# Optimization experiments

Measured on AMD Instinct MI355X. Metric: run time of the kernel, lower is better.

Reference implementation:

```python
import jax, jax.numpy as jnp
import numpy as np

BETA = 0.5
TAU_L = 0.1
TAU_H = 0.1
TOP_K = 2


def setup_inputs() -> dict:
    key = jax.random.key(0)
    ks = jax.random.split(key, 6)
    B, S, H, F, E, NH = 1, 2048, 1024, 3584, 8, 16
    hidden_states = jax.random.normal(ks[0], (B, S, H), dtype=jnp.float32)
    self_attn_weights = jax.random.uniform(ks[1], (B, NH, S, S), dtype=jnp.float32)
    gate_w = jax.random.normal(ks[2], (E, H), dtype=jnp.float32) * 0.02
    w1 = jax.random.normal(ks[3], (E, F, H), dtype=jnp.float32) * 0.02
    w2 = jax.random.normal(ks[4], (E, H, F), dtype=jnp.float32) * 0.02
    w3 = jax.random.normal(ks[5], (E, F, H), dtype=jnp.float32) * 0.02
    return {"hidden_states": hidden_states, "self_attn_weights": self_attn_weights,
            "gate_w": gate_w, "w1": w1, "w2": w2, "w3": w3}


def reference(hidden_states, self_attn_weights, gate_w, w1, w2, w3):
    B, S, H = hidden_states.shape
    E = gate_w.shape[0]
    x = hidden_states.reshape(-1, H)          # [T, H], T = B*S
    T = x.shape[0]

    router_logits = x @ gate_w.T              # [T, E]
    rw_full = jax.nn.softmax(router_logits.astype(jnp.float32), axis=-1)
    rw, sel = jax.lax.top_k(rw_full, TOP_K)   # [T, 2]

    # --- dynamic pruning branch (loss_index < block_range) ---
    mask_top1 = rw[:, 1] < BETA * rw[:, 0]
    new_routing = jnp.ones_like(rw)
    new_routing = new_routing.at[:, 1].set(jnp.where(mask_top1, 0.0, 1.0))

    # sequence_length > 1: attention-based token pruning (assumes B == 1)
    mean_tensor = jnp.mean(jnp.squeeze(self_attn_weights), axis=0)  # [S, S]
    column = mean_tensor.shape[1]
    real_number = jnp.arange(column, 0, -1, dtype=jnp.float32)
    attention_scores = jnp.sum(mean_tensor, axis=1) / real_number   # [S]
    l1_norm = jnp.sum(jnp.abs(x), axis=1)                           # [T]
    attention_scores = attention_scores * l1_norm

    n_low = int(TAU_L * T)
    n_high = int(TAU_H * T)
    _, low_idx = jax.lax.top_k(-attention_scores, n_low)   # smallest
    _, high_idx = jax.lax.top_k(attention_scores, n_high)  # largest
    mask_all = jnp.zeros((T,), dtype=bool).at[low_idx].set(True)
    keep_all = jnp.zeros((T,), dtype=bool).at[high_idx].set(True)
    new_routing = jnp.where(mask_all[:, None], 0.0, new_routing)
    new_routing = jnp.where(keep_all[:, None], 1.0, new_routing)

    rw = rw * new_routing
    denom = jnp.sum(rw, axis=-1, keepdims=True)
    rw = rw / jnp.where(denom > 0, denom, 1.0)  # fully-masked tokens -> 0 output
    rw = rw.astype(x.dtype)

    # combine weights per (token, expert); dispatch mask == new_routing
    cw = jnp.sum(rw[:, :, None] * jax.nn.one_hot(sel, E, dtype=rw.dtype), axis=1)  # [T, E]

    # dense reference for the gather-expert-scatter loop (SwiGLU experts)
    h = jnp.einsum('th,efh->tef', x, w1)      # [T, E, F]
    g = jnp.einsum('th,efh->tef', x, w3)
    a = jax.nn.silu(h) * g
    y = jnp.einsum('tef,ehf->teh', a, w2)     # [T, E, H]
    out = jnp.einsum('te,teh->th', cw, y)     # [T, H]

    return out.reshape(B, S, H), router_logits
```

## Files before the change

### kernel.cpp

```cpp
#include <hip/hip_runtime.h>
#include <hip/hip_bf16.h>
#include <math.h>

#define NTOK 2048
#define HDIM 1024
#define NEXP 8
#define FDIM 3584
#define NHEADS 16
#define NLOW 204
#define NHIGH 204
#define BK 32
#define LDST 40
#define KSPLIT 4
#define KCH (FDIM / KSPLIT)

typedef __bf16 bf16x8 __attribute__((ext_vector_type(8)));
typedef float f32x4 __attribute__((ext_vector_type(4)));

__global__ __launch_bounds__(256) void k_router(
    const float* __restrict__ x, const float* __restrict__ gw,
    float* __restrict__ logits, float* __restrict__ l1,
    int* __restrict__ sel0, int* __restrict__ sel1,
    float* __restrict__ rw0, float* __restrict__ rw1)
{
    __shared__ float sgw[NEXP * HDIM];
    int tid = threadIdx.x;
    for (int i = tid; i < NEXP * HDIM; i += 256) sgw[i] = gw[i];
    __syncthreads();
    int wv = tid >> 6, lane = tid & 63;
    int t = blockIdx.x * 4 + wv;
    const float* xr = x + (size_t)t * HDIM;
    float acc[NEXP];
#pragma unroll
    for (int e = 0; e < NEXP; ++e) acc[e] = 0.f;
    float al1 = 0.f;
    for (int h = lane; h < HDIM; h += 64) {
        float xv = xr[h];
        al1 += fabsf(xv);
#pragma unroll
        for (int e = 0; e < NEXP; ++e) acc[e] += xv * sgw[e * HDIM + h];
    }
#pragma unroll
    for (int off = 32; off > 0; off >>= 1) {
#pragma unroll
        for (int e = 0; e < NEXP; ++e) acc[e] += __shfl_xor(acc[e], off);
        al1 += __shfl_xor(al1, off);
    }
    if (lane < NEXP) logits[t * NEXP + lane] = acc[lane];
    if (lane == 0) {
        l1[t] = al1;
        float m = acc[0];
#pragma unroll
        for (int e = 1; e < NEXP; ++e) m = fmaxf(m, acc[e]);
        float p[NEXP], s = 0.f;
#pragma unroll
        for (int e = 0; e < NEXP; ++e) { p[e] = expf(acc[e] - m); s += p[e]; }
        float inv = 1.f / s;
        float b0 = -1.f, b1 = -1.f; int i0 = 0, i1 = 0;
#pragma unroll
        for (int e = 0; e < NEXP; ++e) {
            float r = p[e] * inv;
            if (r > b0) { b1 = b0; i1 = i0; b0 = r; i0 = e; }
            else if (r > b1) { b1 = r; i1 = e; }
        }
        sel0[t] = i0; sel1[t] = i1; rw0[t] = b0; rw1[t] = b1;
    }
}

__global__ __launch_bounds__(256) void k_attn(
    const float* __restrict__ attn, const float* __restrict__ l1,
    float* __restrict__ scores)
{
    int i = blockIdx.x, tid = threadIdx.x;
    float acc = 0.f;
    for (int h = 0; h < NHEADS; ++h) {
        const float4* p = (const float4*)(attn + ((size_t)h * NTOK + i) * NTOK);
        for (int j = tid; j < NTOK / 4; j += 256) {
            float4 v = p[j];
            acc += v.x + v.y + v.z + v.w;
        }
    }
    __shared__ float red[256];
    red[tid] = acc; __syncthreads();
    for (int s = 128; s > 0; s >>= 1) {
        if (tid < s) red[tid] += red[tid + s];
        __syncthreads();
    }
    if (tid == 0) scores[i] = red[0] / (16.f * (float)(NTOK - i)) * l1[i];
}

__global__ __launch_bounds__(256) void k_rank(
    const float* __restrict__ scores, const float* __restrict__ rw0,
    const float* __restrict__ rw1, float* __restrict__ w0f, float* __restrict__ w1f)
{
    __shared__ float s[NTOK];
    int tid = threadIdx.x;
    for (int i = tid; i < NTOK; i += 256) s[i] = scores[i];
    __syncthreads();
    int t = blockIdx.x * 256 + tid;
    float st = s[t];
    int cl = 0, ch = 0;
    for (int j = 0; j < NTOK; ++j) {
        float sj = s[j];
        int tie = (sj == st) && (j < t);
        cl += (sj < st) || tie;
        ch += (sj > st) || tie;
    }
    bool in_low = cl < NLOW, keep = ch < NHIGH;
    float a = rw0[t], b = rw1[t];
    float n0 = 1.f, n1 = (b < 0.5f * a) ? 0.f : 1.f;
    if (in_low) { n0 = 0.f; n1 = 0.f; }
    if (keep)   { n0 = 1.f; n1 = 1.f; }
    a *= n0; b *= n1;
    float d = a + b;
    if (d > 0.f) { a /= d; b /= d; }
    w0f[t] = a; w1f[t] = b;
}

__global__ __launch_bounds__(512) void k_build(
    const int* __restrict__ sel0, const int* __restrict__ sel1,
    const float* __restrict__ w0f, const float* __restrict__ w1f,
    int* __restrict__ tok, float* __restrict__ wgt,
    int* __restrict__ counts, int* __restrict__ offs)
{
    int tid = threadIdx.x;
    int e = tid >> 6, lane = tid & 63;
    unsigned long long below = (1ull << lane) - 1ull;
    int base = 0;
    for (int r = 0; r < NTOK / 64; ++r) {
        int t = r * 64 + lane;
        bool f0 = (sel0[t] == e) && (w0f[t] > 0.f);
        unsigned long long m0 = __ballot(f0);
        if (f0) {
            int pos = base + __popcll(m0 & below);
            tok[e * NTOK + pos] = t; wgt[e * NTOK + pos] = w0f[t];
        }
        base += __popcll(m0);
        bool f1 = (sel1[t] == e) && (w1f[t] > 0.f);
        unsigned long long m1 = __ballot(f1);
        if (f1) {
            int pos = base + __popcll(m1 & below);
            tok[e * NTOK + pos] = t; wgt[e * NTOK + pos] = w1f[t];
        }
        base += __popcll(m1);
    }
    if (lane == 0) counts[e] = base;
    __syncthreads();
    if (tid == 0) {
        int o = 0;
        for (int i = 0; i < NEXP; ++i) { offs[i] = o; o += counts[i]; }
    }
}

__global__ __launch_bounds__(256) void k_zero(float4* __restrict__ out)
{
    out[blockIdx.x * 256 + threadIdx.x] = make_float4(0.f, 0.f, 0.f, 0.f);
}

struct F16v { float4 a, b, c, d; };
__device__ inline F16v ld16(const float* __restrict__ p)
{
    F16v v;
    v.a = *(const float4*)p;
    v.b = *(const float4*)(p + 4);
    v.c = *(const float4*)(p + 8);
    v.d = *(const float4*)(p + 12);
    return v;
}
__device__ inline void st16(__hip_bfloat16* dst, const F16v& v)
{
    bf16x8 lo, hi;
    lo[0] = (__bf16)v.a.x; lo[1] = (__bf16)v.a.y; lo[2] = (__bf16)v.a.z; lo[3] = (__bf16)v.a.w;
    lo[4] = (__bf16)v.b.x; lo[5] = (__bf16)v.b.y; lo[6] = (__bf16)v.b.z; lo[7] = (__bf16)v.b.w;
    hi[0] = (__bf16)v.c.x; hi[1] = (__bf16)v.c.y; hi[2] = (__bf16)v.c.z; hi[3] = (__bf16)v.c.w;
    hi[4] = (__bf16)v.d.x; hi[5] = (__bf16)v.d.y; hi[6] = (__bf16)v.d.z; hi[7] = (__bf16)v.d.w;
    *(bf16x8*)dst = lo;
    *(bf16x8*)(dst + 8) = hi;
}

__global__ __launch_bounds__(256, 2) void k_ffn1(
    const float* __restrict__ x, const float* __restrict__ w1,
    const float* __restrict__ w3,
    const int* __restrict__ tok, const float* __restrict__ wgt,
    const int* __restrict__ counts, const int* __restrict__ offs,
    __hip_bfloat16* __restrict__ act)
{
    int e = blockIdx.z;
    int cnt = counts[e];
    int m0 = blockIdx.y * 128;
    if (m0 >= cnt) return;
    int f0 = blockIdx.x * 128;
    int tid = threadIdx.x;
    __shared__ __align__(16) __hip_bfloat16 sX[2][128 * LDST];
    __shared__ __align__(16) __hip_bfloat16 sW1[2][128 * LDST];
    __shared__ __align__(16) __hip_bfloat16 sW3[2][128 * LDST];
    __shared__ int sTok[128];
    __shared__ float sWgt[128];
    if (tid < 128) {
        int row = m0 + tid;
        int rr = (row < cnt) ? row : (cnt - 1);
        sTok[tid] = tok[e * NTOK + rr];
        sWgt[tid] = (row < cnt) ? wgt[e * NTOK + row] : 0.f;
    }
    __syncthreads();

    int r = tid >> 1, c16 = (tid & 1) * 16;
    const float* xp  = x  + (size_t)sTok[r] * HDIM + c16;
    const float* w1p = w1 + ((size_t)e * FDIM + f0 + r) * HDIM + c16;
    const float* w3p = w3 + ((size_t)e * FDIM + f0 + r) * HDIM + c16;
    int sidx = r * LDST + c16;

    F16v va = ld16(xp), vb = ld16(w1p), vc = ld16(w3p);
    st16(&sX[0][sidx], va); st16(&sW1[0][sidx], vb); st16(&sW3[0][sidx], vc);
    __syncthreads();

    int wv = tid >> 6, lane = tid & 63;
    int wm = (wv >> 1) * 64, wf = (wv & 1) * 64;
    int col = lane & 15, kfrag = (lane >> 4) * 8;
    f32x4 acc1[4][4] = {}, acc3[4][4] = {};
    int cur = 0;
    for (int k0 = 0; k0 < HDIM; k0 += BK) {
        bool more = (k0 + BK) < HDIM;
        if (more) {
            va = ld16(xp + k0 + BK);
            vb = ld16(w1p + k0 + BK);
            vc = ld16(w3p + k0 + BK);
        }
        bf16x8 af[4], b1[4], b3[4];
#pragma unroll
        for (int m = 0; m < 4; ++m)
            af[m] = *(const bf16x8*)&sX[cur][(wm + m * 16 + col) * LDST + kfrag];
#pragma unroll
        for (int f = 0; f < 4; ++f) {
            b1[f] = *(const bf16x8*)&sW1[cur][(wf + f * 16 + col) * LDST + kfrag];
            b3[f] = *(const bf16x8*)&sW3[cur][(wf + f * 16 + col) * LDST + kfrag];
        }
#pragma unroll
        for (int m = 0; m < 4; ++m)
#pragma unroll
            for (int f = 0; f < 4; ++f) {
                acc1[m][f] = __builtin_amdgcn_mfma_f32_16x16x32_bf16(af[m], b1[f], acc1[m][f], 0, 0, 0);
                acc3[m][f] = __builtin_amdgcn_mfma_f32_16x16x32_bf16(af[m], b3[f], acc3[m][f], 0, 0, 0);
            }
        if (more) {
            st16(&sX[cur ^ 1][sidx], va);
            st16(&sW1[cur ^ 1][sidx], vb);
            st16(&sW3[cur ^ 1][sidx], vc);
        }
        __syncthreads();
        cur ^= 1;
    }
    int soff = offs[e];
#pragma unroll
    for (int m = 0; m < 4; ++m) {
        int mb = wm + m * 16 + (lane >> 4) * 4;
#pragma unroll
        for (int q = 0; q < 4; ++q) {
            int rloc = mb + q;
            if (m0 + rloc < cnt) {
                float wgtv = sWgt[rloc];
#pragma unroll
                for (int f = 0; f < 4; ++f) {
                    float hv = acc1[m][f][q], gv = acc3[m][f][q];
                    float av = hv / (1.f + expf(-hv)) * gv * wgtv;
                    act[(size_t)(soff + m0 + rloc) * FDIM + f0 + wf + f * 16 + col] =
                        (__hip_bfloat16)av;
                }
            }
        }
    }
}

__global__ __launch_bounds__(256, 3) void k_ffn2(
    const __hip_bfloat16* __restrict__ act, const float* __restrict__ w2,
    const int* __restrict__ tok, const int* __restrict__ counts,
    const int* __restrict__ offs, float* __restrict__ out)
{
    int z = blockIdx.z;
    int e = z >> 2;
    int kbase = (z & 3) * KCH;
    int cnt = counts[e];
    int m0 = blockIdx.y * 128;
    if (m0 >= cnt) return;
    int h0 = blockIdx.x * 128;
    int tid = threadIdx.x;
    __shared__ __align__(16) __hip_bfloat16 sA[2][128 * LDST];
    __shared__ __align__(16) __hip_bfloat16 sB[2][128 * LDST];
    __shared__ int sTok[128];
    if (tid < 128) {
        int row = m0 + tid;
        sTok[tid] = (row < cnt) ? tok[e * NTOK + row] : 0;
    }
    __syncthreads();
    int soff = offs[e];
    int r = tid >> 1, c16 = (tid & 1) * 16;
    int arow = (m0 + r < cnt) ? (m0 + r) : (cnt - 1);
    const __hip_bfloat16* ap = act + (size_t)(soff + arow) * FDIM + kbase + c16;
    const float* bp = w2 + ((size_t)e * HDIM + h0 + r) * FDIM + kbase + c16;
    int sidx = r * LDST + c16;

    bf16x8 a0 = *(const bf16x8*)ap, a1 = *(const bf16x8*)(ap + 8);
    F16v vb = ld16(bp);
    *(bf16x8*)&sA[0][sidx] = a0; *(bf16x8*)&sA[0][sidx + 8] = a1;
    st16(&sB[0][sidx], vb);
    __syncthreads();

    int wv = tid >> 6, lane = tid & 63;
    int wm = (wv >> 1) * 64, wh = (wv & 1) * 64;
    int col = lane & 15, kfrag = (lane >> 4) * 8;
    f32x4 acc[4][4] = {};
    int cur = 0;
    for (int k0 = 0; k0 < KCH; k0 += BK) {
        bool more = (k0 + BK) < KCH;
        if (more) {
            a0 = *(const bf16x8*)(ap + k0 + BK);
            a1 = *(const bf16x8*)(ap + k0 + BK + 8);
            vb = ld16(bp + k0 + BK);
        }
        bf16x8 aa[4], bb[4];
#pragma unroll
        for (int m = 0; m < 4; ++m)
            aa[m] = *(const bf16x8*)&sA[cur][(wm + m * 16 + col) * LDST + kfrag];
#pragma unroll
        for (int f = 0; f < 4; ++f)
            bb[f] = *(const bf16x8*)&sB[cur][(wh + f * 16 + col) * LDST + kfrag];
#pragma unroll
        for (int m = 0; m < 4; ++m)
#pragma unroll
            for (int f = 0; f < 4; ++f)
                acc[m][f] = __builtin_amdgcn_mfma_f32_16x16x32_bf16(aa[m], bb[f], acc[m][f], 0, 0, 0);
        if (more) {
            *(bf16x8*)&sA[cur ^ 1][sidx] = a0;
            *(bf16x8*)&sA[cur ^ 1][sidx + 8] = a1;
            st16(&sB[cur ^ 1][sidx], vb);
        }
        __syncthreads();
        cur ^= 1;
    }
#pragma unroll
    for (int m = 0; m < 4; ++m) {
        int mb = wm + m * 16 + (lane >> 4) * 4;
#pragma unroll
        for (int q = 0; q < 4; ++q) {
            int rloc = mb + q;
            if (m0 + rloc < cnt) {
                int t = sTok[rloc];
#pragma unroll
                for (int f = 0; f < 4; ++f)
                    atomicAdd(&out[(size_t)t * HDIM + h0 + wh + f * 16 + col], acc[m][f][q]);
            }
        }
    }
}

extern "C" void kernel_launch(void* const* d_in, const int* in_sizes, int n_in,
                              void* d_out, int out_size, void* d_ws, size_t ws_size,
                              hipStream_t stream)
{
    const float* x    = (const float*)d_in[0];
    const float* attn = (const float*)d_in[1];
    const float* gw   = (const float*)d_in[2];
    const float* w1   = (const float*)d_in[3];
    const float* w2   = (const float*)d_in[4];
    const float* w3   = (const float*)d_in[5];
    float* out = (float*)d_out;
    float* logits = out + (size_t)NTOK * HDIM;

    char* ws = (char*)d_ws;
    float* l1     = (float*)(ws + 0);
    float* scores = (float*)(ws + 8192);
    int*   sel0   = (int*)(ws + 16384);
    int*   sel1   = (int*)(ws + 24576);
    float* rw0    = (float*)(ws + 32768);
    float* rw1    = (float*)(ws + 40960);
    float* w0f    = (float*)(ws + 49152);
    float* w1f    = (float*)(ws + 57344);
    int*   counts = (int*)(ws + 65536);
    int*   offs   = (int*)(ws + 65600);
    int*   tok    = (int*)(ws + 73728);
    float* wgt    = (float*)(ws + 143360);
    __hip_bfloat16* act = (__hip_bfloat16*)(ws + 1048576);

    k_router<<<NTOK / 4, 256, 0, stream>>>(x, gw, logits, l1, sel0, sel1, rw0, rw1);
    k_attn<<<NTOK, 256, 0, stream>>>(attn, l1, scores);
    k_rank<<<NEXP, 256, 0, stream>>>(scores, rw0, rw1, w0f, w1f);
    k_build<<<1, 512, 0, stream>>>(sel0, sel1, w0f, w1f, tok, wgt, counts, offs);
    k_zero<<<NTOK, 256, 0, stream>>>((float4*)out);
    k_ffn1<<<dim3(FDIM / 128, NTOK / 128, NEXP), 256, 0, stream>>>(
        x, w1, w3, tok, wgt, counts, offs, act);
    k_ffn2<<<dim3(HDIM / 128, NTOK / 128, NEXP * KSPLIT), 256, 0, stream>>>(
        act, w2, tok, counts, offs, out);
}
```

Before: 408.4 us.

## Pre-convert activations to bf16 and deepen global-load prefetch in expert GEMMs

Adds a kernel that converts hidden states to bf16 once, so the FFN1 gather loads half the bytes and skips per-tile conversion. Both FFN GEMMs now keep two K-tiles of global loads in flight (a register ping-pong) instead of one, to hide memory latency. The launch grid of k_rank also changes. The deeper prefetch raises register pressure under the two-blocks-per-CU launch bound and may cause spills.

Result: slower. 550.0 us (+34.7%).

```diff
diff --git a/kernel.cpp b/kernel.cpp
--- a/kernel.cpp
+++ b/kernel.cpp
@@ -17,6 +17,18 @@
 typedef __bf16 bf16x8 __attribute__((ext_vector_type(8)));
 typedef float f32x4 __attribute__((ext_vector_type(4)));
 
+__global__ __launch_bounds__(256) void k_xbf16(
+    const float* __restrict__ x, __hip_bfloat16* __restrict__ xb)
+{
+    int i = (blockIdx.x * 256 + threadIdx.x) * 8;
+    float4 a = *(const float4*)(x + i);
+    float4 b = *(const float4*)(x + i + 4);
+    bf16x8 v;
+    v[0] = (__bf16)a.x; v[1] = (__bf16)a.y; v[2] = (__bf16)a.z; v[3] = (__bf16)a.w;
+    v[4] = (__bf16)b.x; v[5] = (__bf16)b.y; v[6] = (__bf16)b.z; v[7] = (__bf16)b.w;
+    *(bf16x8*)(xb + i) = v;
+}
+
 __global__ __launch_bounds__(256) void k_router(
     const float* __restrict__ x, const float* __restrict__ gw,
     float* __restrict__ logits, float* __restrict__ l1,
@@ -179,7 +191,7 @@
 }
 
 __global__ __launch_bounds__(256, 2) void k_ffn1(
-    const float* __restrict__ x, const float* __restrict__ w1,
+    const __hip_bfloat16* __restrict__ xb, const float* __restrict__ w1,
     const float* __restrict__ w3,
     const int* __restrict__ tok, const float* __restrict__ wgt,
     const int* __restrict__ counts, const int* __restrict__ offs,
@@ -205,47 +217,76 @@
     __syncthreads();
 
     int r = tid >> 1, c16 = (tid & 1) * 16;
-    const float* xp  = x  + (size_t)sTok[r] * HDIM + c16;
+    const __hip_bfloat16* xp = xb + (size_t)sTok[r] * HDIM + c16;
     const float* w1p = w1 + ((size_t)e * FDIM + f0 + r) * HDIM + c16;
     const float* w3p = w3 + ((size_t)e * FDIM + f0 + r) * HDIM + c16;
     int sidx = r * LDST + c16;
 
-    F16v va = ld16(xp), vb = ld16(w1p), vc = ld16(w3p);
-    st16(&sX[0][sidx], va); st16(&sW1[0][sidx], vb); st16(&sW3[0][sidx], vc);
+    {
+        bf16x8 x0 = *(const bf16x8*)xp, x1 = *(const bf16x8*)(xp + 8);
+        F16v w0 = ld16(w1p), g0 = ld16(w3p);
+        *(bf16x8*)&sX[0][sidx] = x0;
+        *(bf16x8*)&sX[0][sidx + 8] = x1;
+        st16(&sW1[0][sidx], w0);
+        st16(&sW3[0][sidx], g0);
+    }
+    bf16x8 xB0 = *(const bf16x8*)(xp + BK), xB1 = *(const bf16x8*)(xp + BK + 8);
+    F16v wB = ld16(w1p + BK), gB = ld16(w3p + BK);
     __syncthreads();
 
     int wv = tid >> 6, lane = tid & 63;
     int wm = (wv >> 1) * 64, wf = (wv & 1) * 64;
     int col = lane & 15, kfrag = (lane >> 4) * 8;
     f32x4 acc1[4][4] = {}, acc3[4][4] = {};
+
+    auto compute = [&](int bufi) {
+        bf16x8 af[4], b1f[4], b3f[4];
+#pragma unroll
+        for (int m = 0; m < 4; ++m)
+            af[m] = *(const bf16x8*)&sX[bufi][(wm + m * 16 + col) * LDST + kfrag];
+#pragma unroll
+        for (int f = 0; f < 4; ++f) {
+            b1f[f] = *(const bf16x8*)&sW1[bufi][(wf + f * 16 + col) * LDST + kfrag];
+            b3f[f] = *(const bf16x8*)&sW3[bufi][(wf + f * 16 + col) * LDST + kfrag];
+        }
+#pragma unroll
+        for (int m = 0; m < 4; ++m)
+#pragma unroll
+            for (int f = 0; f < 4; ++f) {
+                acc1[m][f] = __builtin_amdgcn_mfma_f32_16x16x32_bf16(af[m], b1f[f], acc1[m][f], 0, 0, 0);
+                acc3[m][f] = __builtin_amdgcn_mfma_f32_16x16x32_bf16(af[m], b3f[f], acc3[m][f], 0, 0, 0);
+            }
+    };
+
+    bf16x8 xA0, xA1; F16v wA, gA;
     int cur = 0;
-    for (int k0 = 0; k0 < HDIM; k0 += BK) {
-        bool more = (k0 + BK) < HDIM;
-        if (more) {
-            va = ld16(xp + k0 + BK);
-            vb = ld16(w1p + k0 + BK);
-            vc = ld16(w3p + k0 + BK);
-        }
-        bf16x8 af[4], b1[4], b3[4];
-#pragma unroll
-        for (int m = 0; m < 4; ++m)
-            af[m] = *(const bf16x8*)&sX[cur][(wm + m * 16 + col) * LDST + kfrag];
-#pragma unroll
-        for (int f = 0; f < 4; ++f) {
-            b1[f] = *(const bf16x8*)&sW1[cur][(wf + f * 16 + col) * LDST + kfrag];
-            b3[f] = *(const bf16x8*)&sW3[cur][(wf + f * 16 + col) * LDST + kfrag];
-        }
-#pragma unroll
-        for (int m = 0; m < 4; ++m)
-#pragma unroll
-            for (int f = 0; f < 4; ++f) {
-                acc1[m][f] = __builtin_amdgcn_mfma_f32_16x16x32_bf16(af[m], b1[f], acc1[m][f], 0, 0, 0);
-                acc3[m][f] = __builtin_amdgcn_mfma_f32_16x16x32_bf16(af[m], b3[f], acc3[m][f], 0, 0, 0);
-            }
-        if (more) {
-            st16(&sX[cur ^ 1][sidx], va);
-            st16(&sW1[cur ^ 1][sidx], vb);
-            st16(&sW3[cur ^ 1][sidx], vc);
+    for (int i = 0; i < HDIM / BK; i += 2) {
+        const int kc = i * BK;
+        if (i + 2 < HDIM / BK) {
+            xA0 = *(const bf16x8*)(xp + kc + 2 * BK);
+            xA1 = *(const bf16x8*)(xp + kc + 2 * BK + 8);
+            wA = ld16(w1p + kc + 2 * BK);
+            gA = ld16(w3p + kc + 2 * BK);
+        }
+        compute(cur);
+        *(bf16x8*)&sX[cur ^ 1][sidx] = xB0;
+        *(bf16x8*)&sX[cur ^ 1][sidx + 8] = xB1;
+        st16(&sW1[cur ^ 1][sidx], wB);
+        st16(&sW3[cur ^ 1][sidx], gB);
+        __syncthreads();
+        cur ^= 1;
+        if (i + 3 < HDIM / BK) {
+            xB0 = *(const bf16x8*)(xp + kc + 3 * BK);
+            xB1 = *(const bf16x8*)(xp + kc + 3 * BK + 8);
+            wB = ld16(w1p + kc + 3 * BK);
+            gB = ld16(w3p + kc + 3 * BK);
+        }
+        compute(cur);
+        if (i + 2 < HDIM / BK) {
+            *(bf16x8*)&sX[cur ^ 1][sidx] = xA0;
+            *(bf16x8*)&sX[cur ^ 1][sidx + 8] = xA1;
+            st16(&sW1[cur ^ 1][sidx], wA);
+            st16(&sW3[cur ^ 1][sidx], gA);
         }
         __syncthreads();
         cur ^= 1;
@@ -299,40 +340,62 @@
     const float* bp = w2 + ((size_t)e * HDIM + h0 + r) * FDIM + kbase + c16;
     int sidx = r * LDST + c16;
 
-    bf16x8 a0 = *(const bf16x8*)ap, a1 = *(const bf16x8*)(ap + 8);
-    F16v vb = ld16(bp);
-    *(bf16x8*)&sA[0][sidx] = a0; *(bf16x8*)&sA[0][sidx + 8] = a1;
-    st16(&sB[0][sidx], vb);
+    {
+        bf16x8 a0 = *(const bf16x8*)ap, a1 = *(const bf16x8*)(ap + 8);
+        F16v b0 = ld16(bp);
+        *(bf16x8*)&sA[0][sidx] = a0;
+        *(bf16x8*)&sA[0][sidx + 8] = a1;
+        st16(&sB[0][sidx], b0);
+    }
+    bf16x8 aB0 = *(const bf16x8*)(ap + BK), aB1 = *(const bf16x8*)(ap + BK + 8);
+    F16v wB = ld16(bp + BK);
     __syncthreads();
 
     int wv = tid >> 6, lane = tid & 63;
     int wm = (wv >> 1) * 64, wh = (wv & 1) * 64;
     int col = lane & 15, kfrag = (lane >> 4) * 8;
     f32x4 acc[4][4] = {};
-    int cur = 0;
-    for (int k0 = 0; k0 < KCH; k0 += BK) {
-        bool more = (k0 + BK) < KCH;
-        if (more) {
-            a0 = *(const bf16x8*)(ap + k0 + BK);
-            a1 = *(const bf16x8*)(ap + k0 + BK + 8);
-            vb = ld16(bp + k0 + BK);
-        }
+
+    auto compute = [&](int bufi) {
         bf16x8 aa[4], bb[4];
 #pragma unroll
         for (int m = 0; m < 4; ++m)
-            aa[m] = *(const bf16x8*)&sA[cur][(wm + m * 16 + col) * LDST + kfrag];
+            aa[m] = *(const bf16x8*)&sA[bufi][(wm + m * 16 + col) * LDST + kfrag];
 #pragma unroll
         for (int f = 0; f < 4; ++f)
-            bb[f] = *(const bf16x8*)&sB[cur][(wh + f * 16 + col) * LDST + kfrag];
+            bb[f] = *(const bf16x8*)&sB[bufi][(wh + f * 16 + col) * LDST + kfrag];
 #pragma unroll
         for (int m = 0; m < 4; ++m)
 #pragma unroll
             for (int f = 0; f < 4; ++f)
                 acc[m][f] = __builtin_amdgcn_mfma_f32_16x16x32_bf16(aa[m], bb[f], acc[m][f], 0, 0, 0);
-        if (more) {
-            *(bf16x8*)&sA[cur ^ 1][sidx] = a0;
-            *(bf16x8*)&sA[cur ^ 1][sidx + 8] = a1;
-            st16(&sB[cur ^ 1][sidx], vb);
+    };
+
+    bf16x8 aA0, aA1; F16v wA;
+    int cur = 0;
+    for (int i = 0; i < KCH / BK; i += 2) {
+        const int kc = i * BK;
+        if (i + 2 < KCH / BK) {
+            aA0 = *(const bf16x8*)(ap + kc + 2 * BK);
+            aA1 = *(const bf16x8*)(ap + kc + 2 * BK + 8);
+            wA = ld16(bp + kc + 2 * BK);
+        }
+        compute(cur);
+        *(bf16x8*)&sA[cur ^ 1][sidx] = aB0;
+        *(bf16x8*)&sA[cur ^ 1][sidx + 8] = aB1;
+        st16(&sB[cur ^ 1][sidx], wB);
+        __syncthreads();
+        cur ^= 1;
+        if (i + 3 < KCH / BK) {
+            aB0 = *(const bf16x8*)(ap + kc + 3 * BK);
+            aB1 = *(const bf16x8*)(ap + kc + 3 * BK + 8);
+            wB = ld16(bp + kc + 3 * BK);
+        }
+        compute(cur);
+        if (i + 2 < KCH / BK) {
+            *(bf16x8*)&sA[cur ^ 1][sidx] = aA0;
+            *(bf16x8*)&sA[cur ^ 1][sidx + 8] = aA1;
+            st16(&sB[cur ^ 1][sidx], wA);
         }
         __syncthreads();
         cur ^= 1;
@@ -380,14 +443,16 @@
     int*   tok    = (int*)(ws + 73728);
     float* wgt    = (float*)(ws + 143360);
     __hip_bfloat16* act = (__hip_bfloat16*)(ws + 1048576);
-
+    __hip_bfloat16* xb  = (__hip_bfloat16*)(ws + 33554432);
+
+    k_xbf16<<<NTOK * HDIM / (256 * 8), 256, 0, stream>>>(x, xb);
     k_router<<<NTOK / 4, 256, 0, stream>>>(x, gw, logits, l1, sel0, sel1, rw0, rw1);
     k_attn<<<NTOK, 256, 0, stream>>>(attn, l1, scores);
-    k_rank<<<NEXP, 256, 0, stream>>>(scores, rw0, rw1, w0f, w1f);
+    k_rank<<<NTOK / 256, 256, 0, stream>>>(scores, rw0, rw1, w0f, w1f);
     k_build<<<1, 512, 0, stream>>>(sel0, sel1, w0f, w1f, tok, wgt, counts, offs);
     k_zero<<<NTOK, 256, 0, stream>>>((float4*)out);
     k_ffn1<<<dim3(FDIM / 128, NTOK / 128, NEXP), 256, 0, stream>>>(
-        x, w1, w3, tok, wgt, counts, offs, act);
+        xb, w1, w3, tok, wgt, counts, offs, act);
     k_ffn2<<<dim3(HDIM / 128, NTOK / 128, NEXP * KSPLIT), 256, 0, stream>>>(
         act, w2, tok, counts, offs, out);
 }
```

## Split fused gate/up GEMM into two kernels and pre-convert x to bf16

Applied to the files above, without the earlier changes.

Splits the fused w1/w3 expert GEMM into two kernels, k_h and k_g, each with a single accumulator set and a single weight tile. This lowers register and LDS pressure so launch bounds can rise from 2 to 3 blocks per SM. The up kernel writes h to a bf16 buffer that the gate kernel reads back in its SiLU epilogue. x is converted to bf16 once up front, so gathered token rows are loaded as bf16 and each x tile is loaded twice instead of once. This adds an extra kernel launch and an h round trip through global memory. The k_rank grid also changes from NEXP to NTOK/256, which is the same value (8).

Result: slower. 474.9 us (+16.3%).

```diff
diff --git a/kernel.cpp b/kernel.cpp
--- a/kernel.cpp
+++ b/kernel.cpp
@@ -17,6 +17,18 @@
 typedef __bf16 bf16x8 __attribute__((ext_vector_type(8)));
 typedef float f32x4 __attribute__((ext_vector_type(4)));
 
+__global__ __launch_bounds__(256) void k_xbf16(
+    const float* __restrict__ x, __hip_bfloat16* __restrict__ xb)
+{
+    int i = (blockIdx.x * 256 + threadIdx.x) * 8;
+    float4 a = *(const float4*)(x + i);
+    float4 b = *(const float4*)(x + i + 4);
+    bf16x8 v;
+    v[0] = (__bf16)a.x; v[1] = (__bf16)a.y; v[2] = (__bf16)a.z; v[3] = (__bf16)a.w;
+    v[4] = (__bf16)b.x; v[5] = (__bf16)b.y; v[6] = (__bf16)b.z; v[7] = (__bf16)b.w;
+    *(bf16x8*)(xb + i) = v;
+}
+
 __global__ __launch_bounds__(256) void k_router(
     const float* __restrict__ x, const float* __restrict__ gw,
     float* __restrict__ logits, float* __restrict__ l1,
@@ -178,12 +190,10 @@
     *(bf16x8*)(dst + 8) = hi;
 }
 
-__global__ __launch_bounds__(256, 2) void k_ffn1(
-    const float* __restrict__ x, const float* __restrict__ w1,
-    const float* __restrict__ w3,
-    const int* __restrict__ tok, const float* __restrict__ wgt,
-    const int* __restrict__ counts, const int* __restrict__ offs,
-    __hip_bfloat16* __restrict__ act)
+__global__ __launch_bounds__(256, 3) void k_h(
+    const __hip_bfloat16* __restrict__ xb, const float* __restrict__ w1,
+    const int* __restrict__ tok, const int* __restrict__ counts,
+    const int* __restrict__ offs, __hip_bfloat16* __restrict__ hbuf)
 {
     int e = blockIdx.z;
     int cnt = counts[e];
@@ -192,8 +202,93 @@
     int f0 = blockIdx.x * 128;
     int tid = threadIdx.x;
     __shared__ __align__(16) __hip_bfloat16 sX[2][128 * LDST];
-    __shared__ __align__(16) __hip_bfloat16 sW1[2][128 * LDST];
-    __shared__ __align__(16) __hip_bfloat16 sW3[2][128 * LDST];
+    __shared__ __align__(16) __hip_bfloat16 sW[2][128 * LDST];
+    __shared__ int sTok[128];
+    if (tid < 128) {
+        int row = m0 + tid;
+        int rr = (row < cnt) ? row : (cnt - 1);
+        sTok[tid] = tok[e * NTOK + rr];
+    }
+    __syncthreads();
+
+    int r = tid >> 1, c16 = (tid & 1) * 16;
+    const __hip_bfloat16* xp = xb + (size_t)sTok[r] * HDIM + c16;
+    const float* wp = w1 + ((size_t)e * FDIM + f0 + r) * HDIM + c16;
+    int sidx = r * LDST + c16;
+
+    {
+        bf16x8 x0 = *(const bf16x8*)xp, x1 = *(const bf16x8*)(xp + 8);
+        F16v w0 = ld16(wp);
+        *(bf16x8*)&sX[0][sidx] = x0;
+        *(bf16x8*)&sX[0][sidx + 8] = x1;
+        st16(&sW[0][sidx], w0);
+    }
+    __syncthreads();
+
+    int wv = tid >> 6, lane = tid & 63;
+    int wm = (wv >> 1) * 64, wf = (wv & 1) * 64;
+    int col = lane & 15, kfrag = (lane >> 4) * 8;
+    f32x4 acc[4][4] = {};
+    int cur = 0;
+    for (int k0 = 0; k0 < HDIM; k0 += BK) {
+        bool more = (k0 + BK) < HDIM;
+        bf16x8 xn0, xn1; F16v wn;
+        if (more) {
+            xn0 = *(const bf16x8*)(xp + k0 + BK);
+            xn1 = *(const bf16x8*)(xp + k0 + BK + 8);
+            wn = ld16(wp + k0 + BK);
+        }
+        bf16x8 aa[4], bb[4];
+#pragma unroll
+        for (int m = 0; m < 4; ++m)
+            aa[m] = *(const bf16x8*)&sX[cur][(wm + m * 16 + col) * LDST + kfrag];
+#pragma unroll
+        for (int f = 0; f < 4; ++f)
+            bb[f] = *(const bf16x8*)&sW[cur][(wf + f * 16 + col) * LDST + kfrag];
+#pragma unroll
+        for (int m = 0; m < 4; ++m)
+#pragma unroll
+            for (int f = 0; f < 4; ++f)
+                acc[m][f] = __builtin_amdgcn_mfma_f32_16x16x32_bf16(aa[m], bb[f], acc[m][f], 0, 0, 0);
+        if (more) {
+            *(bf16x8*)&sX[cur ^ 1][sidx] = xn0;
+            *(bf16x8*)&sX[cur ^ 1][sidx + 8] = xn1;
+            st16(&sW[cur ^ 1][sidx], wn);
+        }
+        __syncthreads();
+        cur ^= 1;
+    }
+    int soff = offs[e];
+#pragma unroll
+    for (int m = 0; m < 4; ++m) {
+        int mb = wm + m * 16 + (lane >> 4) * 4;
+#pragma unroll
+        for (int q = 0; q < 4; ++q) {
+            int rloc = mb + q;
+            if (m0 + rloc < cnt) {
+#pragma unroll
+                for (int f = 0; f < 4; ++f)
+                    hbuf[(size_t)(soff + m0 + rloc) * FDIM + f0 + wf + f * 16 + col] =
+                        (__hip_bfloat16)acc[m][f][q];
+            }
+        }
+    }
+}
+
+__global__ __launch_bounds__(256, 3) void k_g(
+    const __hip_bfloat16* __restrict__ xb, const float* __restrict__ w3,
+    const int* __restrict__ tok, const float* __restrict__ wgt,
+    const int* __restrict__ counts, const int* __restrict__ offs,
+    const __hip_bfloat16* __restrict__ hbuf, __hip_bfloat16* __restrict__ act)
+{
+    int e = blockIdx.z;
+    int cnt = counts[e];
+    int m0 = blockIdx.y * 128;
+    if (m0 >= cnt) return;
+    int f0 = blockIdx.x * 128;
+    int tid = threadIdx.x;
+    __shared__ __align__(16) __hip_bfloat16 sX[2][128 * LDST];
+    __shared__ __align__(16) __hip_bfloat16 sW[2][128 * LDST];
     __shared__ int sTok[128];
     __shared__ float sWgt[128];
     if (tid < 128) {
@@ -205,47 +300,48 @@
     __syncthreads();
 
     int r = tid >> 1, c16 = (tid & 1) * 16;
-    const float* xp  = x  + (size_t)sTok[r] * HDIM + c16;
-    const float* w1p = w1 + ((size_t)e * FDIM + f0 + r) * HDIM + c16;
-    const float* w3p = w3 + ((size_t)e * FDIM + f0 + r) * HDIM + c16;
+    const __hip_bfloat16* xp = xb + (size_t)sTok[r] * HDIM + c16;
+    const float* wp = w3 + ((size_t)e * FDIM + f0 + r) * HDIM + c16;
     int sidx = r * LDST + c16;
 
-    F16v va = ld16(xp), vb = ld16(w1p), vc = ld16(w3p);
-    st16(&sX[0][sidx], va); st16(&sW1[0][sidx], vb); st16(&sW3[0][sidx], vc);
+    {
+        bf16x8 x0 = *(const bf16x8*)xp, x1 = *(const bf16x8*)(xp + 8);
+        F16v w0 = ld16(wp);
+        *(bf16x8*)&sX[0][sidx] = x0;
+        *(bf16x8*)&sX[0][sidx + 8] = x1;
+        st16(&sW[0][sidx], w0);
+    }
     __syncthreads();
 
     int wv = tid >> 6, lane = tid & 63;
     int wm = (wv >> 1) * 64, wf = (wv & 1) * 64;
     int col = lane & 15, kfrag = (lane >> 4) * 8;
-    f32x4 acc1[4][4] = {}, acc3[4][4] = {};
+    f32x4 acc[4][4] = {};
     int cur = 0;
     for (int k0 = 0; k0 < HDIM; k0 += BK) {
         bool more = (k0 + BK) < HDIM;
-        if (more) {
-            va = ld16(xp + k0 + BK);
-            vb = ld16(w1p + k0 + BK);
-            vc = ld16(w3p + k0 + BK);
-        }
-        bf16x8 af[4], b1[4], b3[4];
-#pragma unroll
-        for (int m = 0; m < 4; ++m)
-            af[m] = *(const bf16x8*)&sX[cur][(wm + m * 16 + col) * LDST + kfrag];
-#pragma unroll
-        for (int f = 0; f < 4; ++f) {
-            b1[f] = *(const bf16x8*)&sW1[cur][(wf + f * 16 + col) * LDST + kfrag];
-            b3[f] = *(const bf16x8*)&sW3[cur][(wf + f * 16 + col) * LDST + kfrag];
-        }
-#pragma unroll
-        for (int m = 0; m < 4; ++m)
-#pragma unroll
-            for (int f = 0; f < 4; ++f) {
-                acc1[m][f] = __builtin_amdgcn_mfma_f32_16x16x32_bf16(af[m], b1[f], acc1[m][f], 0, 0, 0);
-                acc3[m][f] = __builtin_amdgcn_mfma_f32_16x16x32_bf16(af[m], b3[f], acc3[m][f], 0, 0, 0);
-            }
-        if (more) {
-            st16(&sX[cur ^ 1][sidx], va);
-            st16(&sW1[cur ^ 1][sidx], vb);
-            st16(&sW3[cur ^ 1][sidx], vc);
+        bf16x8 xn0, xn1; F16v wn;
+        if (more) {
+            xn0 = *(const bf16x8*)(xp + k0 + BK);
+            xn1 = *(const bf16x8*)(xp + k0 + BK + 8);
+            wn = ld16(wp + k0 + BK);
+        }
+        bf16x8 aa[4], bb[4];
+#pragma unroll
+        for (int m = 0; m < 4; ++m)
+            aa[m] = *(const bf16x8*)&sX[cur][(wm + m * 16 + col) * LDST + kfrag];
+#pragma unroll
+        for (int f = 0; f < 4; ++f)
+            bb[f] = *(const bf16x8*)&sW[cur][(wf + f * 16 + col) * LDST + kfrag];
+#pragma unroll
+        for (int m = 0; m < 4; ++m)
+#pragma unroll
+            for (int f = 0; f < 4; ++f)
+                acc[m][f] = __builtin_amdgcn_mfma_f32_16x16x32_bf16(aa[m], bb[f], acc[m][f], 0, 0, 0);
+        if (more) {
+            *(bf16x8*)&sX[cur ^ 1][sidx] = xn0;
+            *(bf16x8*)&sX[cur ^ 1][sidx + 8] = xn1;
+            st16(&sW[cur ^ 1][sidx], wn);
         }
         __syncthreads();
         cur ^= 1;
@@ -259,12 +355,13 @@
             int rloc = mb + q;
             if (m0 + rloc < cnt) {
                 float wgtv = sWgt[rloc];
+                size_t base = (size_t)(soff + m0 + rloc) * FDIM + f0 + wf + col;
 #pragma unroll
                 for (int f = 0; f < 4; ++f) {
-                    float hv = acc1[m][f][q], gv = acc3[m][f][q];
+                    float hv = (float)hbuf[base + f * 16];
+                    float gv = acc[m][f][q];
                     float av = hv / (1.f + expf(-hv)) * gv * wgtv;
-                    act[(size_t)(soff + m0 + rloc) * FDIM + f0 + wf + f * 16 + col] =
-                        (__hip_bfloat16)av;
+                    act[base + f * 16] = (__hip_bfloat16)av;
                 }
             }
         }
@@ -299,10 +396,13 @@
     const float* bp = w2 + ((size_t)e * HDIM + h0 + r) * FDIM + kbase + c16;
     int sidx = r * LDST + c16;
 
-    bf16x8 a0 = *(const bf16x8*)ap, a1 = *(const bf16x8*)(ap + 8);
-    F16v vb = ld16(bp);
-    *(bf16x8*)&sA[0][sidx] = a0; *(bf16x8*)&sA[0][sidx + 8] = a1;
-    st16(&sB[0][sidx], vb);
+    {
+        bf16x8 a0 = *(const bf16x8*)ap, a1 = *(const bf16x8*)(ap + 8);
+        F16v b0 = ld16(bp);
+        *(bf16x8*)&sA[0][sidx] = a0;
+        *(bf16x8*)&sA[0][sidx + 8] = a1;
+        st16(&sB[0][sidx], b0);
+    }
     __syncthreads();
 
     int wv = tid >> 6, lane = tid & 63;
@@ -312,10 +412,11 @@
     int cur = 0;
     for (int k0 = 0; k0 < KCH; k0 += BK) {
         bool more = (k0 + BK) < KCH;
-        if (more) {
-            a0 = *(const bf16x8*)(ap + k0 + BK);
-            a1 = *(const bf16x8*)(ap + k0 + BK + 8);
-            vb = ld16(bp + k0 + BK);
+        bf16x8 an0, an1; F16v wn;
+        if (more) {
+            an0 = *(const bf16x8*)(ap + k0 + BK);
+            an1 = *(const bf16x8*)(ap + k0 + BK + 8);
+            wn = ld16(bp + k0 + BK);
         }
         bf16x8 aa[4], bb[4];
 #pragma unroll
@@ -330,9 +431,9 @@
             for (int f = 0; f < 4; ++f)
                 acc[m][f] = __builtin_amdgcn_mfma_f32_16x16x32_bf16(aa[m], bb[f], acc[m][f], 0, 0, 0);
         if (more) {
-            *(bf16x8*)&sA[cur ^ 1][sidx] = a0;
-            *(bf16x8*)&sA[cur ^ 1][sidx + 8] = a1;
-            st16(&sB[cur ^ 1][sidx], vb);
+            *(bf16x8*)&sA[cur ^ 1][sidx] = an0;
+            *(bf16x8*)&sA[cur ^ 1][sidx + 8] = an1;
+            st16(&sB[cur ^ 1][sidx], wn);
         }
         __syncthreads();
         cur ^= 1;
@@ -379,15 +480,20 @@
     int*   offs   = (int*)(ws + 65600);
     int*   tok    = (int*)(ws + 73728);
     float* wgt    = (float*)(ws + 143360);
-    __hip_bfloat16* act = (__hip_bfloat16*)(ws + 1048576);
-
+    __hip_bfloat16* act  = (__hip_bfloat16*)(ws + 1048576);
+    __hip_bfloat16* xb   = (__hip_bfloat16*)(ws + 33554432);
+    __hip_bfloat16* hbuf = (__hip_bfloat16*)(ws + 67108864);
+
+    k_xbf16<<<NTOK * HDIM / (256 * 8), 256, 0, stream>>>(x, xb);
     k_router<<<NTOK / 4, 256, 0, stream>>>(x, gw, logits, l1, sel0, sel1, rw0, rw1);
     k_attn<<<NTOK, 256, 0, stream>>>(attn, l1, scores);
-    k_rank<<<NEXP, 256, 0, stream>>>(scores, rw0, rw1, w0f, w1f);
+    k_rank<<<NTOK / 256, 256, 0, stream>>>(scores, rw0, rw1, w0f, w1f);
     k_build<<<1, 512, 0, stream>>>(sel0, sel1, w0f, w1f, tok, wgt, counts, offs);
     k_zero<<<NTOK, 256, 0, stream>>>((float4*)out);
-    k_ffn1<<<dim3(FDIM / 128, NTOK / 128, NEXP), 256, 0, stream>>>(
-        x, w1, w3, tok, wgt, counts, offs, act);
+    k_h<<<dim3(FDIM / 128, NTOK / 128, NEXP), 256, 0, stream>>>(
+        xb, w1, tok, counts, offs, hbuf);
+    k_g<<<dim3(FDIM / 128, NTOK / 128, NEXP), 256, 0, stream>>>(
+        xb, w3, tok, wgt, counts, offs, hbuf, act);
     k_ffn2<<<dim3(HDIM / 128, NTOK / 128, NEXP * KSPLIT), 256, 0, stream>>>(
         act, w2, tok, counts, offs, out);
 }
```
